# Kernel tuning notes

Hardware: AMD Instinct MI355X
Metric: run time of the kernel (lower is better)

## Reference

```python
import jax, jax.numpy as jnp
import numpy as np

N = 50000


def gcn_conv(x, edge_index, W, b):
    # PyG GCNConv: h = XW; add self-loops; sym-normalized scatter-add; + bias
    n = x.shape[0]
    h = x @ W  # [N, out]
    loop = jnp.arange(n)
    src = jnp.concatenate([edge_index[0], loop])
    dst = jnp.concatenate([edge_index[1], loop])
    deg = jax.ops.segment_sum(jnp.ones_like(dst, dtype=h.dtype), dst, num_segments=n)
    dinv = jax.lax.rsqrt(jnp.maximum(deg, 1.0))  # deg >= 1 after self-loops
    norm = dinv[src] * dinv[dst]  # [E+N]
    msg = h[src] * norm[:, None]  # [E+N, out]
    return jax.ops.segment_sum(msg, dst, num_segments=n) + b


def setup_inputs() -> dict:
    key = jax.random.key(0)
    ks = jax.random.split(key, 20)
    E = 1600000
    inp = {
        "metadata_a": jax.random.normal(ks[0], (N, 512), jnp.float32),
        "metadata_b": jax.random.normal(ks[1], (N, 512), jnp.float32),
        "x_a": jax.random.normal(ks[2], (N, 256), jnp.float32),
        "x_b": jax.random.normal(ks[3], (N, 256), jnp.float32),
        "edge_index_a": jax.random.randint(ks[4], (2, E), 0, N, dtype=jnp.int64),
        "edge_index_b": jax.random.randint(ks[5], (2, E), 0, N, dtype=jnp.int64),
        # parameters (fan-in scaled)
        "fc1_W": jax.random.normal(ks[6], (512, 128), jnp.float32) / np.sqrt(512),
        "fc1_b": jnp.zeros((128,), jnp.float32),
        "fc2_W": jax.random.normal(ks[7], (128, 128), jnp.float32) / np.sqrt(128),
        "fc2_b": jnp.zeros((128,), jnp.float32),
        "gcn1_W": jax.random.normal(ks[8], (256, 128), jnp.float32) / np.sqrt(256),
        "gcn1_b": jnp.zeros((128,), jnp.float32),
        "gcn2_W": jax.random.normal(ks[9], (128, 128), jnp.float32) / np.sqrt(128),
        "gcn2_b": jnp.zeros((128,), jnp.float32),
        "fcc_W": jax.random.normal(ks[10], (512, 128), jnp.float32) / np.sqrt(512),
        "fcc_b": jnp.zeros((128,), jnp.float32),
        "out_W": jax.random.normal(ks[11], (128, 1), jnp.float32) / np.sqrt(128),
        "out_b": jnp.zeros((1,), jnp.float32),
    }
    return inp


def reference(metadata_a, metadata_b, x_a, x_b, edge_index_a, edge_index_b,
              fc1_W, fc1_b, fc2_W, fc2_b, gcn1_W, gcn1_b, gcn2_W, gcn2_b,
              fcc_W, fcc_b, out_W, out_b):
    def mlp(m):
        m = jax.nn.relu(m @ fc1_W + fc1_b)
        return jax.nn.relu(m @ fc2_W + fc2_b)

    def gcn_branch(x, ei):
        x = jax.nn.relu(gcn_conv(x, ei, gcn1_W, gcn1_b))
        return jax.nn.relu(gcn_conv(x, ei, gcn2_W, gcn2_b))

    ma = mlp(metadata_a)
    mb = mlp(metadata_b)
    ga = gcn_branch(x_a, edge_index_a)
    gb = gcn_branch(x_b, edge_index_b)
    combined = jnp.concatenate([ma, mb, ga, gb], axis=1)  # [N, 512]
    combined = jax.nn.relu(combined @ fcc_W + fcc_b)
    return jax.nn.sigmoid(combined @ out_W + out_b)  # [N, 1]
```

## Files before the change

kernel.cpp:

```cpp
#include <hip/hip_runtime.h>
#include <math.h>


typedef __attribute__((ext_vector_type(8))) short bf16x8;
typedef __attribute__((ext_vector_type(4))) float f32x4;

static __device__ __forceinline__ unsigned short f2bf(float f) {
  unsigned u = __float_as_uint(f);
  unsigned r = u + 0x7fffu + ((u >> 16) & 1u);
  return (unsigned short)(r >> 16);
}
static __device__ __forceinline__ float bflo(unsigned m) { return __uint_as_float(m << 16); }
static __device__ __forceinline__ float bfhi(unsigned m) { return __uint_as_float(m & 0xffff0000u); }

static __device__ __forceinline__ bf16x8 cvt8(const float4& l, const float4& h) {
  bf16x8 a;
  a[0] = (short)f2bf(l.x); a[1] = (short)f2bf(l.y);
  a[2] = (short)f2bf(l.z); a[3] = (short)f2bf(l.w);
  a[4] = (short)f2bf(h.x); a[5] = (short)f2bf(h.y);
  a[6] = (short)f2bf(h.z); a[7] = (short)f2bf(h.w);
  return a;
}

template <int AFP32>
__launch_bounds__(256)
__global__ void gemm_mfma(const void* __restrict__ Av, const void* __restrict__ Av2,
                          int lda, const unsigned short* __restrict__ Wt,
                          const float* __restrict__ bias, const float* __restrict__ rowscale,
                          unsigned short* __restrict__ Cb, unsigned short* __restrict__ Cb2,
                          int ldc, int co, int co2, int Mh, int M, int K, int do_relu) {
  const int tid = threadIdx.x;
  const int wave = tid >> 6, lane = tid & 63, quad = lane >> 4, lr = lane & 15;
  const int m0 = blockIdx.x * 64 + wave * 16;

  f32x4 acc[8];
#pragma unroll
  for (int c = 0; c < 8; c++) acc[c] = (f32x4){0.f, 0.f, 0.f, 0.f};

  int rg = m0 + lr; if (rg > M - 1) rg = M - 1;
  const int h = rg >= Mh;
  const size_t rl = (size_t)(rg - (h ? Mh : 0));
  const int KT = K >> 5;

  const bf16x8* Bf = (const bf16x8*)Wt + lane;
  const float* apf = (const float*)(h ? Av2 : Av) + rl * lda + quad * 8;
  const unsigned short* aph = (const unsigned short*)(h ? Av2 : Av) + rl * lda + quad * 8;

  float4 pl[2], ph[2];
  bf16x8 pa[2];
  if (AFP32) {
    pl[0] = *(const float4*)apf; ph[0] = *(const float4*)(apf + 4);
    if (KT > 1) { pl[1] = *(const float4*)(apf + 32); ph[1] = *(const float4*)(apf + 36); }
  } else {
    pa[0] = *(const bf16x8*)aph;
    if (KT > 1) pa[1] = *(const bf16x8*)(aph + 32);
  }
  bf16x8 bc[8], bn[8];
#pragma unroll
  for (int c = 0; c < 8; c++) bc[c] = Bf[c * 64];

  for (int kt = 0; kt < KT; kt++) {
    bf16x8 a;
    if (AFP32) a = cvt8(pl[kt & 1], ph[kt & 1]);
    else       a = pa[kt & 1];
    if (kt + 2 < KT) {
      if (AFP32) {
        const float* pp = apf + (size_t)(kt + 2) * 32;
        pl[kt & 1] = *(const float4*)pp; ph[kt & 1] = *(const float4*)(pp + 4);
      } else {
        pa[kt & 1] = *(const bf16x8*)(aph + (size_t)(kt + 2) * 32);
      }
    }
    if (kt + 1 < KT) {
      const bf16x8* Bk = Bf + (size_t)(kt + 1) * 512;
#pragma unroll
      for (int c = 0; c < 8; c++) bn[c] = Bk[c * 64];
    }
#pragma unroll
    for (int c = 0; c < 8; c++)
      acc[c] = __builtin_amdgcn_mfma_f32_16x16x32_bf16(a, bc[c], acc[c], 0, 0, 0);
    if (kt + 1 < KT) {
#pragma unroll
      for (int c = 0; c < 8; c++) bc[c] = bn[c];
    }
  }

  const int rbase = m0 + quad * 4;
  float rs[4];
#pragma unroll
  for (int i = 0; i < 4; i++) {
    int row = rbase + i;
    rs[i] = (rowscale && row < M) ? rowscale[row] : 1.0f;
  }
#pragma unroll
  for (int c = 0; c < 8; c++) {
    const int nc = c * 16 + lr;
    const float bi = bias ? bias[nc] : 0.f;
#pragma unroll
    for (int i = 0; i < 4; i++) {
      int row = rbase + i;
      if (row < M) {
        int hh = row >= Mh;
        int rr = row - (hh ? Mh : 0);
        float v = acc[c][i] * rs[i] + bi;
        if (do_relu) v = fmaxf(v, 0.f);
        unsigned short* C = hh ? Cb2 : Cb;
        C[(size_t)rr * ldc + (hh ? co2 : co) + nc] = f2bf(v);
      }
    }
  }
}

__launch_bounds__(256)
__global__ void gemm_head(const unsigned short* __restrict__ A,
                          const unsigned short* __restrict__ Wt,
                          const float* __restrict__ bias,
                          const float* __restrict__ outW, const float* __restrict__ outb,
                          float* __restrict__ y, int M) {
  const int tid = threadIdx.x;
  const int wave = tid >> 6, lane = tid & 63, quad = lane >> 4, lr = lane & 15;
  const int m0 = blockIdx.x * 64 + wave * 16;

  f32x4 acc[8];
#pragma unroll
  for (int c = 0; c < 8; c++) acc[c] = (f32x4){0.f, 0.f, 0.f, 0.f};

  int rg = m0 + lr; if (rg > M - 1) rg = M - 1;
  const unsigned short* aph = A + (size_t)rg * 512 + quad * 8;
  const int KT = 16;
  const bf16x8* Bf = (const bf16x8*)Wt + lane;

  bf16x8 pa[2];
  pa[0] = *(const bf16x8*)aph;
  pa[1] = *(const bf16x8*)(aph + 32);
  bf16x8 bc[8], bn[8];
#pragma unroll
  for (int c = 0; c < 8; c++) bc[c] = Bf[c * 64];

  for (int kt = 0; kt < KT; kt++) {
    bf16x8 a = pa[kt & 1];
    if (kt + 2 < KT) pa[kt & 1] = *(const bf16x8*)(aph + (size_t)(kt + 2) * 32);
    if (kt + 1 < KT) {
      const bf16x8* Bk = Bf + (size_t)(kt + 1) * 512;
#pragma unroll
      for (int c = 0; c < 8; c++) bn[c] = Bk[c * 64];
    }
#pragma unroll
    for (int c = 0; c < 8; c++)
      acc[c] = __builtin_amdgcn_mfma_f32_16x16x32_bf16(a, bc[c], acc[c], 0, 0, 0);
    if (kt + 1 < KT) {
#pragma unroll
      for (int c = 0; c < 8; c++) bc[c] = bn[c];
    }
  }

  float part[4] = {0.f, 0.f, 0.f, 0.f};
#pragma unroll
  for (int c = 0; c < 8; c++) {
    const int nc = c * 16 + lr;
    float w = outW[nc];
    float bi = bias[nc];
#pragma unroll
    for (int i = 0; i < 4; i++) part[i] += fmaxf(acc[c][i] + bi, 0.f) * w;
  }
#pragma unroll
  for (int i = 0; i < 4; i++) {
    part[i] += __shfl_xor(part[i], 1, 64);
    part[i] += __shfl_xor(part[i], 2, 64);
    part[i] += __shfl_xor(part[i], 4, 64);
    part[i] += __shfl_xor(part[i], 8, 64);
  }
  if (lr == 0) {
    const float ob = outb[0];
#pragma unroll
    for (int i = 0; i < 4; i++) {
      int row = m0 + quad * 4 + i;
      if (row < M) y[row] = 1.f / (1.f + expf(-(part[i] + ob)));
    }
  }
}

__global__ void prep_w(const float* __restrict__ fc1, const float* __restrict__ fc2,
                       const float* __restrict__ g1, const float* __restrict__ g2,
                       const float* __restrict__ fcc, unsigned short* __restrict__ wt) {
  int t = blockIdx.x * 256 + threadIdx.x;
  const float* src[5] = {fc1, fc2, g1, g2, fcc};
  const int Ks[5] = {512, 128, 256, 128, 512};
  int off = 0;
#pragma unroll
  for (int w = 0; w < 5; w++) {
    int K = Ks[w];
    int ngroups = K * 16;
    if (t < ngroups) {
      int lane = t & 63;
      int c = (t >> 6) & 7;
      int kt = t >> 9;
      int quad = lane >> 4, lr = lane & 15;
      int n = c * 16 + lr;
      unsigned short* dst = wt + off + (size_t)t * 8;
      const float* s = src[w];
#pragma unroll
      for (int j = 0; j < 8; j++) {
        int k = kt * 32 + quad * 8 + j;
        dst[j] = f2bf(s[k * 128 + n]);
      }
    }
    off += K * 128;
  }
}

__global__ void init_csr(int* __restrict__ gcur, int NB, int BCAP) {
  int i = blockIdx.x * 256 + threadIdx.x;
  if (i < 2 * NB) gcur[i] = i * BCAP;
}

__launch_bounds__(256)
__global__ void bucket_scatter(const int* __restrict__ eiA, const int* __restrict__ eiB,
                               int E, int T, int NB, int* __restrict__ gcur,
                               unsigned* __restrict__ records) {
  __shared__ unsigned staging[4096];
  __shared__ int hist[129];
  __shared__ int offs[129];
  __shared__ int gbase[128];
  __shared__ int sm[128];
  const int g = blockIdx.x >= T;
  const int tile = blockIdx.x - g * T;
  const int* ei = g ? eiB : eiA;
  const int tid = threadIdx.x;
  for (int i = tid; i <= NB; i += 256) hist[i] = 0;
  __syncthreads();
  const int base = tile * 4096;
  int myb[16], myp[16];
  unsigned myrec[16];
#pragma unroll
  for (int j = 0; j < 16; j++) {
    int li = base + j * 256 + tid;
    int b = NB;
    unsigned rec = 0;
    if (li < E) {
      int s = ei[li], d = ei[E + li];
      b = d >> 9;
      rec = (unsigned)s | ((unsigned)d << 16);
    }
    myb[j] = b; myrec[j] = rec;
    myp[j] = atomicAdd(&hist[b], 1);
  }
  __syncthreads();
  if (tid < 128) sm[tid] = (tid <= NB) ? hist[tid] : 0;
  __syncthreads();
  for (int d = 1; d < 128; d <<= 1) {
    int v = 0;
    if (tid < 128) { v = sm[tid]; if (tid >= d) v += sm[tid - d]; }
    __syncthreads();
    if (tid < 128) sm[tid] = v;
    __syncthreads();
  }
  if (tid < 128) offs[tid] = sm[tid] - ((tid <= NB) ? hist[tid] : 0);
  __syncthreads();
#pragma unroll
  for (int j = 0; j < 16; j++)
    if (myb[j] < NB) staging[offs[myb[j]] + myp[j]] = myrec[j];
  if (tid < NB && hist[tid] > 0) gbase[tid] = atomicAdd(&gcur[g * NB + tid], hist[tid]);
  __syncthreads();
  const int total = offs[NB];
  for (int i = tid; i < total; i += 256) {
    unsigned rec = staging[i];
    int b = (int)(rec >> 16) >> 9;
    records[gbase[b] + (i - offs[b])] = rec;
  }
}

__launch_bounds__(256)
__global__ void csr_build(const unsigned* __restrict__ records, const int* __restrict__ gcur,
                          int N, int NB, int BCAP,
                          int2* __restrict__ rpA, int2* __restrict__ rpB,
                          float* __restrict__ dinv, unsigned short* __restrict__ csrAll) {
  __shared__ int ncnt[512];
  __shared__ int excl[512];
  __shared__ int sm[256];
  const int g = blockIdx.x >= NB;
  const int b = blockIdx.x - g * NB;
  const int tid = threadIdx.x;
  const int R = (g * NB + b) * BCAP;
  const int cnt = gcur[g * NB + b] - R;
  const int node0 = b << 9;
  const int nb = min(512, N - node0);
  const unsigned* rec = records + R;
  int2* rp = g ? rpB : rpA;
  unsigned short* csr = csrAll + (size_t)g * NB * BCAP;

  for (int i = tid; i < 512; i += 256) ncnt[i] = 0;
  __syncthreads();
  for (int i = tid; i < cnt; i += 256)
    atomicAdd(&ncnt[(rec[i] >> 16) & 511], 1);
  __syncthreads();
  int a0 = ncnt[2 * tid], a1 = ncnt[2 * tid + 1];
  int ps = a0 + a1;
  sm[tid] = ps;
  __syncthreads();
  for (int d = 1; d < 256; d <<= 1) {
    int v = sm[tid];
    if (tid >= d) v += sm[tid - d];
    __syncthreads();
    sm[tid] = v;
    __syncthreads();
  }
  int e0 = sm[tid] - ps;
  excl[2 * tid] = e0;
  excl[2 * tid + 1] = e0 + a0;
  __syncthreads();
  for (int i = tid; i < nb; i += 256) {
    int s = b * BCAP + excl[i];
    rp[node0 + i] = make_int2(s, s + ncnt[i]);
    dinv[g * N + node0 + i] = rsqrtf((float)(ncnt[i] + 1));
  }
  __syncthreads();
  for (int i = tid; i < 512; i += 256) ncnt[i] = excl[i];
  __syncthreads();
  for (int i = tid; i < cnt; i += 256) {
    unsigned r = rec[i];
    int p = atomicAdd(&ncnt[(r >> 16) & 511], 1);
    csr[b * BCAP + p] = (unsigned short)(r & 0xffffu);
  }
}

struct f2x4 { float2 a, b, c, d; };
static __device__ __forceinline__ void acc2(f2x4& A, const uint4& m) {
  A.a.x += bflo(m.x); A.a.y += bfhi(m.x);
  A.b.x += bflo(m.y); A.b.y += bfhi(m.y);
  A.c.x += bflo(m.z); A.c.y += bfhi(m.z);
  A.d.x += bflo(m.w); A.d.y += bfhi(m.w);
}

__launch_bounds__(256)
__global__ void gather16(const unsigned short* __restrict__ hsA,
                         const unsigned short* __restrict__ hsB,
                         const unsigned short* __restrict__ csrA,
                         const unsigned short* __restrict__ csrB,
                         const int2* __restrict__ rpA, const int2* __restrict__ rpB,
                         const float* __restrict__ dinv,
                         const float* __restrict__ bias,
                         unsigned short* __restrict__ outA, unsigned short* __restrict__ outB,
                         int ldA, int coA, int ldB, int coB, int N) {
  int widx = (blockIdx.x * 256 + threadIdx.x) >> 6;
  if (widx >= 2 * N) return;
  int g = widx >= N;
  int v = g ? widx - N : widx;
  const unsigned short* hs = g ? hsB : hsA;
  const unsigned short* csr = g ? csrB : csrA;
  int2 se = (g ? rpB : rpA)[v];
  unsigned short* out = g ? outB : outA;
  const int ldc = g ? ldB : ldA;
  const int co = g ? coB : coA;
  const int lane = threadIdx.x & 63;
  const int grp = lane >> 4;
  const int u = lane & 15;
  const unsigned short* rowb = hs + u * 8;

  f2x4 A0 = {{0,0},{0,0},{0,0},{0,0}};
  f2x4 A1 = {{0,0},{0,0},{0,0},{0,0}};

  int e = se.x;
  const int end = se.y;
  for (; e + 16 <= end; e += 16) {
    int s0 = csr[e + grp];
    int s1 = csr[e + 4 + grp];
    int s2 = csr[e + 8 + grp];
    int s3 = csr[e + 12 + grp];
    uint4 m0 = *(const uint4*)(rowb + (size_t)s0 * 128);
    uint4 m1 = *(const uint4*)(rowb + (size_t)s1 * 128);
    uint4 m2 = *(const uint4*)(rowb + (size_t)s2 * 128);
    uint4 m3 = *(const uint4*)(rowb + (size_t)s3 * 128);
    acc2(A0, m0); acc2(A1, m1); acc2(A0, m2); acc2(A1, m3);
  }
  for (; e + 4 <= end; e += 4) {
    int s0 = csr[e + grp];
    uint4 m0 = *(const uint4*)(rowb + (size_t)s0 * 128);
    acc2(A0, m0);
  }
  int r = end - e;
  if (r > 0) {
    int s0 = csr[e + (grp < r ? grp : r - 1)];
    uint4 m = *(const uint4*)(rowb + (size_t)s0 * 128);
    float msk = (grp < r) ? 1.f : 0.f;
    A1.a.x = fmaf(msk, bflo(m.x), A1.a.x); A1.a.y = fmaf(msk, bfhi(m.x), A1.a.y);
    A1.b.x = fmaf(msk, bflo(m.y), A1.b.x); A1.b.y = fmaf(msk, bfhi(m.y), A1.b.y);
    A1.c.x = fmaf(msk, bflo(m.z), A1.c.x); A1.c.y = fmaf(msk, bfhi(m.z), A1.c.y);
    A1.d.x = fmaf(msk, bflo(m.w), A1.d.x); A1.d.y = fmaf(msk, bfhi(m.w), A1.d.y);
  }

  float acc[8] = {A0.a.x + A1.a.x, A0.a.y + A1.a.y, A0.b.x + A1.b.x, A0.b.y + A1.b.y,
                  A0.c.x + A1.c.x, A0.c.y + A1.c.y, A0.d.x + A1.d.x, A0.d.y + A1.d.y};
#pragma unroll
  for (int j = 0; j < 8; j++) {
    acc[j] += __shfl_down(acc[j], 32, 64);
    acc[j] += __shfl_down(acc[j], 16, 64);
  }
  if (grp == 0) {
    uint4 smv = *(const uint4*)(rowb + (size_t)v * 128);
    acc[0] += bflo(smv.x); acc[1] += bfhi(smv.x);
    acc[2] += bflo(smv.y); acc[3] += bfhi(smv.y);
    acc[4] += bflo(smv.z); acc[5] += bfhi(smv.z);
    acc[6] += bflo(smv.w); acc[7] += bfhi(smv.w);
    float dv = dinv[g * N + v];
    float4 b0 = *(const float4*)(bias + u * 8);
    float4 b1 = *(const float4*)(bias + u * 8 + 4);
    float o0 = fmaxf(acc[0] * dv + b0.x, 0.f), o1 = fmaxf(acc[1] * dv + b0.y, 0.f);
    float o2 = fmaxf(acc[2] * dv + b0.z, 0.f), o3 = fmaxf(acc[3] * dv + b0.w, 0.f);
    float o4 = fmaxf(acc[4] * dv + b1.x, 0.f), o5 = fmaxf(acc[5] * dv + b1.y, 0.f);
    float o6 = fmaxf(acc[6] * dv + b1.z, 0.f), o7 = fmaxf(acc[7] * dv + b1.w, 0.f);
    uint4 P;
    P.x = (unsigned)f2bf(o0) | ((unsigned)f2bf(o1) << 16);
    P.y = (unsigned)f2bf(o2) | ((unsigned)f2bf(o3) << 16);
    P.z = (unsigned)f2bf(o4) | ((unsigned)f2bf(o5) << 16);
    P.w = (unsigned)f2bf(o6) | ((unsigned)f2bf(o7) << 16);
    *(uint4*)(out + (size_t)v * ldc + co + u * 8) = P;
  }
}

extern "C" void kernel_launch(void* const* d_in, const int* in_sizes, int n_in,
                              void* d_out, int out_size, void* d_ws, size_t ws_size,
                              hipStream_t stream) {
  const float* meta_a = (const float*)d_in[0];
  const float* meta_b = (const float*)d_in[1];
  const float* x_a    = (const float*)d_in[2];
  const float* x_b    = (const float*)d_in[3];
  const int*   ei_a   = (const int*)d_in[4];
  const int*   ei_b   = (const int*)d_in[5];
  const float* fc1_W = (const float*)d_in[6];
  const float* fc1_b = (const float*)d_in[7];
  const float* fc2_W = (const float*)d_in[8];
  const float* fc2_b = (const float*)d_in[9];
  const float* gcn1_W = (const float*)d_in[10];
  const float* gcn1_b = (const float*)d_in[11];
  const float* gcn2_W = (const float*)d_in[12];
  const float* gcn2_b = (const float*)d_in[13];
  const float* fcc_W = (const float*)d_in[14];
  const float* fcc_b = (const float*)d_in[15];
  const float* out_W = (const float*)d_in[16];
  const float* out_b = (const float*)d_in[17];
  float* y = (float*)d_out;

  const int N = in_sizes[0] / 512;
  const int E = in_sizes[4] / 2;
  const int NB = (N + 511) >> 9;
  const int T = (E + 4095) / 4096;
  const int BCAP = 17408;

  char* p = (char*)d_ws;
  auto alloc = [&](size_t bytes) { char* r = p; p += (bytes + 255) & ~255ull; return r; };
  unsigned short* combined = (unsigned short*)alloc((size_t)N * 512 * 2);
  unsigned short* t0 = (unsigned short*)alloc((size_t)N * 128 * 2);
  unsigned short* t1 = (unsigned short*)alloc((size_t)N * 128 * 2);
  unsigned short* t2 = (unsigned short*)alloc((size_t)N * 128 * 2);
  unsigned short* t3 = (unsigned short*)alloc((size_t)N * 128 * 2);
  unsigned short* wt = (unsigned short*)alloc(196608 * 2);
  float* dinv = (float*)alloc((size_t)2 * N * 4);
  int2* rpA = (int2*)alloc((size_t)N * 8);
  int2* rpB = (int2*)alloc((size_t)N * 8);
  int* gcur = (int*)alloc((size_t)2 * NB * 4);
  unsigned* records = (unsigned*)alloc((size_t)2 * NB * BCAP * 4 + 4096);
  unsigned short* csrAll = (unsigned short*)alloc((size_t)2 * NB * BCAP * 2 + 4096);
  unsigned short* csrA = csrAll;
  unsigned short* csrB = csrAll + (size_t)NB * BCAP;

  unsigned short* wt_fc1 = wt;
  unsigned short* wt_fc2 = wt + 65536;
  unsigned short* wt_g1  = wt + 81920;
  unsigned short* wt_g2  = wt + 114688;
  unsigned short* wt_fcc = wt + 131072;

  const int grid1 = (N + 63) / 64;
  const int grid2 = (2 * N + 63) / 64;

  prep_w<<<32, 256, 0, stream>>>(fc1_W, fc2_W, gcn1_W, gcn2_W, fcc_W, wt);
  init_csr<<<1, 256, 0, stream>>>(gcur, NB, BCAP);
  bucket_scatter<<<2 * T, 256, 0, stream>>>(ei_a, ei_b, E, T, NB, gcur, records);
  csr_build<<<2 * NB, 256, 0, stream>>>(records, gcur, N, NB, BCAP, rpA, rpB, dinv, csrAll);

  gemm_mfma<1><<<grid2, 256, 0, stream>>>(meta_a, meta_b, 512, wt_fc1, fc1_b, nullptr,
                                          t0, t1, 128, 0, 0, N, 2 * N, 512, 1);
  gemm_mfma<0><<<grid2, 256, 0, stream>>>(t0, t1, 128, wt_fc2, fc2_b, nullptr,
                                          combined, combined, 512, 0, 128, N, 2 * N, 128, 1);

  gemm_mfma<1><<<grid2, 256, 0, stream>>>(x_a, x_b, 256, wt_g1, nullptr, dinv,
                                          t0, t1, 128, 0, 0, N, 2 * N, 256, 0);
  gather16<<<(2 * N + 3) / 4, 256, 0, stream>>>(t0, t1, csrA, csrB, rpA, rpB, dinv, gcn1_b,
                                                t2, t3, 128, 0, 128, 0, N);
  gemm_mfma<0><<<grid2, 256, 0, stream>>>(t2, t3, 128, wt_g2, nullptr, dinv,
                                          t0, t1, 128, 0, 0, N, 2 * N, 128, 0);
  gather16<<<(2 * N + 3) / 4, 256, 0, stream>>>(t0, t1, csrA, csrB, rpA, rpB, dinv, gcn2_b,
                                                combined, combined, 512, 256, 512, 384, N);

  gemm_head<<<grid1, 256, 0, stream>>>(combined, wt_fcc, fcc_b, out_W, out_b, y, N);
}
```

Measured before the change: 808.2 us.

## Stage GEMM weights in LDS via async loads and double the rows per wave

Both GEMM kernels now copy each 32-wide K slice of the weight matrix into a double-buffered shared-memory tile using global_load_lds, instead of having every wave load it from global memory into registers. Each wave now computes two 16-row tiles against the same weight fragment, so a block covers 128 rows and the grids are halved. The aim is to cut redundant weight traffic and increase MFMA work per weight load. In exchange it adds a block-wide barrier every K step and roughly doubles accumulator register use, which may lower occupancy.

```diff
diff --git a/kernel.cpp b/kernel.cpp
--- a/kernel.cpp
+++ b/kernel.cpp
@@ -22,6 +22,12 @@
   return a;
 }
 
+static __device__ __forceinline__ void gl_lds16(const unsigned short* g, unsigned short* l) {
+  __builtin_amdgcn_global_load_lds(
+      (const __attribute__((address_space(1))) void*)g,
+      (__attribute__((address_space(3))) void*)l, 16, 0, 0);
+}
+
 template <int AFP32>
 __launch_bounds__(256)
 __global__ void gemm_mfma(const void* __restrict__ Av, const void* __restrict__ Av2,
@@ -29,83 +35,106 @@
                           const float* __restrict__ bias, const float* __restrict__ rowscale,
                           unsigned short* __restrict__ Cb, unsigned short* __restrict__ Cb2,
                           int ldc, int co, int co2, int Mh, int M, int K, int do_relu) {
+  __shared__ unsigned short Bs[2][4096];
   const int tid = threadIdx.x;
   const int wave = tid >> 6, lane = tid & 63, quad = lane >> 4, lr = lane & 15;
-  const int m0 = blockIdx.x * 64 + wave * 16;
-
-  f32x4 acc[8];
-#pragma unroll
-  for (int c = 0; c < 8; c++) acc[c] = (f32x4){0.f, 0.f, 0.f, 0.f};
-
-  int rg = m0 + lr; if (rg > M - 1) rg = M - 1;
-  const int h = rg >= Mh;
-  const size_t rl = (size_t)(rg - (h ? Mh : 0));
+  const int m0 = blockIdx.x * 128 + wave * 32;
   const int KT = K >> 5;
 
-  const bf16x8* Bf = (const bf16x8*)Wt + lane;
-  const float* apf = (const float*)(h ? Av2 : Av) + rl * lda + quad * 8;
-  const unsigned short* aph = (const unsigned short*)(h ? Av2 : Av) + rl * lda + quad * 8;
-
-  float4 pl[2], ph[2];
-  bf16x8 pa[2];
-  if (AFP32) {
-    pl[0] = *(const float4*)apf; ph[0] = *(const float4*)(apf + 4);
-    if (KT > 1) { pl[1] = *(const float4*)(apf + 32); ph[1] = *(const float4*)(apf + 36); }
-  } else {
-    pa[0] = *(const bf16x8*)aph;
-    if (KT > 1) pa[1] = *(const bf16x8*)(aph + 32);
-  }
-  bf16x8 bc[8], bn[8];
-#pragma unroll
-  for (int c = 0; c < 8; c++) bc[c] = Bf[c * 64];
-
+  f32x4 acc[2][8];
+#pragma unroll
+  for (int t = 0; t < 2; t++)
+#pragma unroll
+    for (int c = 0; c < 8; c++) acc[t][c] = (f32x4){0.f, 0.f, 0.f, 0.f};
+
+  const float* apf[2];
+  const unsigned short* aph[2];
+#pragma unroll
+  for (int t = 0; t < 2; t++) {
+    int rg = m0 + t * 16 + lr; if (rg > M - 1) rg = M - 1;
+    const int h = rg >= Mh;
+    const size_t rl = (size_t)(rg - (h ? Mh : 0));
+    if (AFP32) apf[t] = (const float*)(h ? Av2 : Av) + rl * lda + quad * 8;
+    else       aph[t] = (const unsigned short*)(h ? Av2 : Av) + rl * lda + quad * 8;
+  }
+
+  {
+    const unsigned short* g = Wt + wave * 1024 + lane * 8;
+    gl_lds16(g,       &Bs[0][wave * 1024]);
+    gl_lds16(g + 512, &Bs[0][wave * 1024 + 512]);
+  }
+  float4 pl[2][2], ph[2][2];
+  bf16x8 pa[2][2];
+#pragma unroll
+  for (int t = 0; t < 2; t++) {
+    if (AFP32) {
+      pl[t][0] = *(const float4*)apf[t]; ph[t][0] = *(const float4*)(apf[t] + 4);
+      if (KT > 1) { pl[t][1] = *(const float4*)(apf[t] + 32); ph[t][1] = *(const float4*)(apf[t] + 36); }
+    } else {
+      pa[t][0] = *(const bf16x8*)aph[t];
+      if (KT > 1) pa[t][1] = *(const bf16x8*)(aph[t] + 32);
+    }
+  }
+  __syncthreads();
+
+  int buf = 0;
   for (int kt = 0; kt < KT; kt++) {
-    bf16x8 a;
-    if (AFP32) a = cvt8(pl[kt & 1], ph[kt & 1]);
-    else       a = pa[kt & 1];
+    if (kt + 1 < KT) {
+      const unsigned short* g = Wt + (size_t)(kt + 1) * 4096 + wave * 1024 + lane * 8;
+      gl_lds16(g,       &Bs[buf ^ 1][wave * 1024]);
+      gl_lds16(g + 512, &Bs[buf ^ 1][wave * 1024 + 512]);
+    }
+    bf16x8 a[2];
+#pragma unroll
+    for (int t = 0; t < 2; t++) {
+      if (AFP32) a[t] = cvt8(pl[t][kt & 1], ph[t][kt & 1]);
+      else       a[t] = pa[t][kt & 1];
+    }
     if (kt + 2 < KT) {
-      if (AFP32) {
-        const float* pp = apf + (size_t)(kt + 2) * 32;
-        pl[kt & 1] = *(const float4*)pp; ph[kt & 1] = *(const float4*)(pp + 4);
-      } else {
-        pa[kt & 1] = *(const bf16x8*)(aph + (size_t)(kt + 2) * 32);
+#pragma unroll
+      for (int t = 0; t < 2; t++) {
+        if (AFP32) {
+          const float* pp = apf[t] + (size_t)(kt + 2) * 32;
+          pl[t][kt & 1] = *(const float4*)pp; ph[t][kt & 1] = *(const float4*)(pp + 4);
+        } else {
+          pa[t][kt & 1] = *(const bf16x8*)(aph[t] + (size_t)(kt + 2) * 32);
+        }
       }
     }
-    if (kt + 1 < KT) {
-      const bf16x8* Bk = Bf + (size_t)(kt + 1) * 512;
-#pragma unroll
-      for (int c = 0; c < 8; c++) bn[c] = Bk[c * 64];
-    }
-#pragma unroll
-    for (int c = 0; c < 8; c++)
-      acc[c] = __builtin_amdgcn_mfma_f32_16x16x32_bf16(a, bc[c], acc[c], 0, 0, 0);
-    if (kt + 1 < KT) {
-#pragma unroll
-      for (int c = 0; c < 8; c++) bc[c] = bn[c];
-    }
-  }
-
-  const int rbase = m0 + quad * 4;
-  float rs[4];
-#pragma unroll
-  for (int i = 0; i < 4; i++) {
-    int row = rbase + i;
-    rs[i] = (rowscale && row < M) ? rowscale[row] : 1.0f;
-  }
-#pragma unroll
-  for (int c = 0; c < 8; c++) {
-    const int nc = c * 16 + lr;
-    const float bi = bias ? bias[nc] : 0.f;
+#pragma unroll
+    for (int c = 0; c < 8; c++) {
+      bf16x8 b = *(const bf16x8*)&Bs[buf][(c * 64 + lane) * 8];
+      acc[0][c] = __builtin_amdgcn_mfma_f32_16x16x32_bf16(a[0], b, acc[0][c], 0, 0, 0);
+      acc[1][c] = __builtin_amdgcn_mfma_f32_16x16x32_bf16(a[1], b, acc[1][c], 0, 0, 0);
+    }
+    if (kt + 1 < KT) __syncthreads();
+    buf ^= 1;
+  }
+
+#pragma unroll
+  for (int t = 0; t < 2; t++) {
+    const int rbase = m0 + t * 16 + quad * 4;
+    float rs[4];
 #pragma unroll
     for (int i = 0; i < 4; i++) {
       int row = rbase + i;
-      if (row < M) {
-        int hh = row >= Mh;
-        int rr = row - (hh ? Mh : 0);
-        float v = acc[c][i] * rs[i] + bi;
-        if (do_relu) v = fmaxf(v, 0.f);
-        unsigned short* C = hh ? Cb2 : Cb;
-        C[(size_t)rr * ldc + (hh ? co2 : co) + nc] = f2bf(v);
+      rs[i] = (rowscale && row < M) ? rowscale[row] : 1.0f;
+    }
+#pragma unroll
+    for (int c = 0; c < 8; c++) {
+      const int nc = c * 16 + lr;
+      const float bi = bias ? bias[nc] : 0.f;
+#pragma unroll
+      for (int i = 0; i < 4; i++) {
+        int row = rbase + i;
+        if (row < M) {
+          int hh = row >= Mh;
+          int rr = row - (hh ? Mh : 0);
+          float v = acc[t][c][i] * rs[i] + bi;
+          if (do_relu) v = fmaxf(v, 0.f);
+          unsigned short* C = hh ? Cb2 : Cb;
+          C[(size_t)rr * ldc + (hh ? co2 : co) + nc] = f2bf(v);
+        }
       }
     }
   }
@@ -117,66 +146,92 @@
                           const float* __restrict__ bias,
                           const float* __restrict__ outW, const float* __restrict__ outb,
                           float* __restrict__ y, int M) {
+  __shared__ unsigned short Bs[2][4096];
   const int tid = threadIdx.x;
   const int wave = tid >> 6, lane = tid & 63, quad = lane >> 4, lr = lane & 15;
-  const int m0 = blockIdx.x * 64 + wave * 16;
-
-  f32x4 acc[8];
-#pragma unroll
-  for (int c = 0; c < 8; c++) acc[c] = (f32x4){0.f, 0.f, 0.f, 0.f};
-
-  int rg = m0 + lr; if (rg > M - 1) rg = M - 1;
-  const unsigned short* aph = A + (size_t)rg * 512 + quad * 8;
+  const int m0 = blockIdx.x * 128 + wave * 32;
   const int KT = 16;
-  const bf16x8* Bf = (const bf16x8*)Wt + lane;
-
-  bf16x8 pa[2];
-  pa[0] = *(const bf16x8*)aph;
-  pa[1] = *(const bf16x8*)(aph + 32);
-  bf16x8 bc[8], bn[8];
-#pragma unroll
-  for (int c = 0; c < 8; c++) bc[c] = Bf[c * 64];
-
+
+  f32x4 acc[2][8];
+#pragma unroll
+  for (int t = 0; t < 2; t++)
+#pragma unroll
+    for (int c = 0; c < 8; c++) acc[t][c] = (f32x4){0.f, 0.f, 0.f, 0.f};
+
+  const unsigned short* aph[2];
+#pragma unroll
+  for (int t = 0; t < 2; t++) {
+    int rg = m0 + t * 16 + lr; if (rg > M - 1) rg = M - 1;
+    aph[t] = A + (size_t)rg * 512 + quad * 8;
+  }
+
+  {
+    const unsigned short* g = Wt + wave * 1024 + lane * 8;
+    gl_lds16(g,       &Bs[0][wave * 1024]);
+    gl_lds16(g + 512, &Bs[0][wave * 1024 + 512]);
+  }
+  bf16x8 pa[2][2];
+#pragma unroll
+  for (int t = 0; t < 2; t++) {
+    pa[t][0] = *(const bf16x8*)aph[t];
+    pa[t][1] = *(const bf16x8*)(aph[t] + 32);
+  }
+  __syncthreads();
+
+  int buf = 0;
   for (int kt = 0; kt < KT; kt++) {
-    bf16x8 a = pa[kt & 1];
-    if (kt + 2 < KT) pa[kt & 1] = *(const bf16x8*)(aph + (size_t)(kt + 2) * 32);
     if (kt + 1 < KT) {
-      const bf16x8* Bk = Bf + (size_t)(kt + 1) * 512;
-#pragma unroll
-      for (int c = 0; c < 8; c++) bn[c] = Bk[c * 64];
-    }
-#pragma unroll
-    for (int c = 0; c < 8; c++)
-      acc[c] = __builtin_amdgcn_mfma_f32_16x16x32_bf16(a, bc[c], acc[c], 0, 0, 0);
-    if (kt + 1 < KT) {
-#pragma unroll
-      for (int c = 0; c < 8; c++) bc[c] = bn[c];
-    }
-  }
-
-  float part[4] = {0.f, 0.f, 0.f, 0.f};
-#pragma unroll
-  for (int c = 0; c < 8; c++) {
-    const int nc = c * 16 + lr;
-    float w = outW[nc];
-    float bi = bias[nc];
-#pragma unroll
-    for (int i = 0; i < 4; i++) part[i] += fmaxf(acc[c][i] + bi, 0.f) * w;
-  }
-#pragma unroll
-  for (int i = 0; i < 4; i++) {
-    part[i] += __shfl_xor(part[i], 1, 64);
-    part[i] += __shfl_xor(part[i], 2, 64);
-    part[i] += __shfl_xor(part[i], 4, 64);
-    part[i] += __shfl_xor(part[i], 8, 64);
-  }
+      const unsigned short* g = Wt + (size_t)(kt + 1) * 4096 + wave * 1024 + lane * 8;
+      gl_lds16(g,       &Bs[buf ^ 1][wave * 1024]);
+      gl_lds16(g + 512, &Bs[buf ^ 1][wave * 1024 + 512]);
+    }
+    bf16x8 a[2];
+#pragma unroll
+    for (int t = 0; t < 2; t++) a[t] = pa[t][kt & 1];
+    if (kt + 2 < KT) {
+#pragma unroll
+      for (int t = 0; t < 2; t++)
+        pa[t][kt & 1] = *(const bf16x8*)(aph[t] + (size_t)(kt + 2) * 32);
+    }
+#pragma unroll
+    for (int c = 0; c < 8; c++) {
+      bf16x8 b = *(const bf16x8*)&Bs[buf][(c * 64 + lane) * 8];
+      acc[0][c] = __builtin_amdgcn_mfma_f32_16x16x32_bf16(a[0], b, acc[0][c], 0, 0, 0);
+      acc[1][c] = __builtin_amdgcn_mfma_f32_16x16x32_bf16(a[1], b, acc[1][c], 0, 0, 0);
+    }
+    if (kt + 1 < KT) __syncthreads();
+    buf ^= 1;
+  }
+
+  float part[2][4] = {{0.f, 0.f, 0.f, 0.f}, {0.f, 0.f, 0.f, 0.f}};
+#pragma unroll
+  for (int t = 0; t < 2; t++)
+#pragma unroll
+    for (int c = 0; c < 8; c++) {
+      const int nc = c * 16 + lr;
+      float w = outW[nc];
+      float bi = bias[nc];
+#pragma unroll
+      for (int i = 0; i < 4; i++) part[t][i] += fmaxf(acc[t][c][i] + bi, 0.f) * w;
+    }
+#pragma unroll
+  for (int t = 0; t < 2; t++)
+#pragma unroll
+    for (int i = 0; i < 4; i++) {
+      part[t][i] += __shfl_xor(part[t][i], 1, 64);
+      part[t][i] += __shfl_xor(part[t][i], 2, 64);
+      part[t][i] += __shfl_xor(part[t][i], 4, 64);
+      part[t][i] += __shfl_xor(part[t][i], 8, 64);
+    }
   if (lr == 0) {
     const float ob = outb[0];
 #pragma unroll
-    for (int i = 0; i < 4; i++) {
-      int row = m0 + quad * 4 + i;
-      if (row < M) y[row] = 1.f / (1.f + expf(-(part[i] + ob)));
-    }
+    for (int t = 0; t < 2; t++)
+#pragma unroll
+      for (int i = 0; i < 4; i++) {
+        int row = m0 + t * 16 + quad * 4 + i;
+        if (row < M) y[row] = 1.f / (1.f + expf(-(part[t][i] + ob)));
+      }
   }
 }
 
@@ -470,8 +525,8 @@
   unsigned short* wt_g2  = wt + 114688;
   unsigned short* wt_fcc = wt + 131072;
 
-  const int grid1 = (N + 63) / 64;
-  const int grid2 = (2 * N + 63) / 64;
+  const int grid1 = (N + 127) / 128;
+  const int grid2 = (2 * N + 127) / 128;
 
   prep_w<<<32, 256, 0, stream>>>(fc1_W, fc2_W, gcn1_W, gcn2_W, fcc_W, wt);
   init_csr<<<1, 256, 0, stream>>>(gcur, NB, BCAP);
```

After: 965.5 us. 1.19x slower.

## Stage fp32 GEMM inputs through LDS with direct global-to-LDS loads

Applied to the files above, without the earlier changes.

The fp32-input GEMMs (fc1 and gcn1) now stage the A tile into double-buffered shared memory with global_load_lds, using an XOR swizzle, and read it back for bf16 conversion, instead of each lane issuing strided per-row register loads. The K=128 bf16 GEMMs get a specialised kernel that preloads all four A fragments up front. The head GEMM now prefetches A in groups of four k-steps. The aim is better-coalesced, deeper-pipelined reads of the large fp32 activation matrices, at the cost of 64KB of shared memory per block (lower occupancy) and a block barrier per chunk.

```diff
diff --git a/kernel.cpp b/kernel.cpp
--- a/kernel.cpp
+++ b/kernel.cpp
@@ -22,66 +22,86 @@
   return a;
 }
 
-template <int AFP32>
+static __device__ __forceinline__ void gl_lds16(const unsigned short* g, unsigned short* l) {
+  __builtin_amdgcn_global_load_lds(
+      (const __attribute__((address_space(1))) void*)g,
+      (__attribute__((address_space(3))) void*)l, 16, 0, 0);
+}
+
+template <int KT>
 __launch_bounds__(256)
-__global__ void gemm_mfma(const void* __restrict__ Av, const void* __restrict__ Av2,
-                          int lda, const unsigned short* __restrict__ Wt,
-                          const float* __restrict__ bias, const float* __restrict__ rowscale,
-                          unsigned short* __restrict__ Cb, unsigned short* __restrict__ Cb2,
-                          int ldc, int co, int co2, int Mh, int M, int K, int do_relu) {
+__global__ void gemm_staged(const float* __restrict__ Av, const float* __restrict__ Av2,
+                            int lda, const unsigned short* __restrict__ Wt,
+                            const float* __restrict__ bias, const float* __restrict__ rowscale,
+                            unsigned short* __restrict__ Cb, unsigned short* __restrict__ Cb2,
+                            int ldc, int co, int co2, int Mh, int M, int do_relu) {
+  static_assert(KT % 4 == 0, "KT multiple of 4");
+  constexpr int NCH = KT / 4;
+  __shared__ float4 As[2][2048];
   const int tid = threadIdx.x;
   const int wave = tid >> 6, lane = tid & 63, quad = lane >> 4, lr = lane & 15;
   const int m0 = blockIdx.x * 64 + wave * 16;
+  const int mb = blockIdx.x * 64;
 
   f32x4 acc[8];
 #pragma unroll
   for (int c = 0; c < 8; c++) acc[c] = (f32x4){0.f, 0.f, 0.f, 0.f};
 
-  int rg = m0 + lr; if (rg > M - 1) rg = M - 1;
-  const int h = rg >= Mh;
-  const size_t rl = (size_t)(rg - (h ? Mh : 0));
-  const int KT = K >> 5;
+  const int colq_src = (tid & 7) ^ ((tid >> 3) & 7);
+  int r0g = mb + (tid >> 3);      if (r0g > M - 1) r0g = M - 1;
+  int r1g = mb + 32 + (tid >> 3); if (r1g > M - 1) r1g = M - 1;
+  const int h0 = r0g >= Mh, h1 = r1g >= Mh;
+  const float* srcb0 = (h0 ? Av2 : Av) + (size_t)(r0g - (h0 ? Mh : 0)) * lda + colq_src * 4;
+  const float* srcb1 = (h1 ? Av2 : Av) + (size_t)(r1g - (h1 ? Mh : 0)) * lda + colq_src * 4;
+
+  auto stage = [&](int buf, int c0) {
+#pragma unroll
+    for (int s = 0; s < 8; s++) {
+      const float* g = ((s & 1) ? srcb1 : srcb0) + (size_t)(c0 * 4 + (s >> 1)) * 32;
+      gl_lds16((const unsigned short*)g,
+               (unsigned short*)&As[buf][s * 256 + wave * 64]);
+    }
+  };
+
+  const int h32 = wave >> 1;
+  const int r5 = (wave & 1) * 16 + lr;
+  const int swz = r5 & 7;
+  const int fb_ = h32 * 256 + r5 * 8;
 
   const bf16x8* Bf = (const bf16x8*)Wt + lane;
-  const float* apf = (const float*)(h ? Av2 : Av) + rl * lda + quad * 8;
-  const unsigned short* aph = (const unsigned short*)(h ? Av2 : Av) + rl * lda + quad * 8;
-
-  float4 pl[2], ph[2];
-  bf16x8 pa[2];
-  if (AFP32) {
-    pl[0] = *(const float4*)apf; ph[0] = *(const float4*)(apf + 4);
-    if (KT > 1) { pl[1] = *(const float4*)(apf + 32); ph[1] = *(const float4*)(apf + 36); }
-  } else {
-    pa[0] = *(const bf16x8*)aph;
-    if (KT > 1) pa[1] = *(const bf16x8*)(aph + 32);
-  }
-  bf16x8 bc[8], bn[8];
-#pragma unroll
-  for (int c = 0; c < 8; c++) bc[c] = Bf[c * 64];
-
-  for (int kt = 0; kt < KT; kt++) {
-    bf16x8 a;
-    if (AFP32) a = cvt8(pl[kt & 1], ph[kt & 1]);
-    else       a = pa[kt & 1];
-    if (kt + 2 < KT) {
-      if (AFP32) {
-        const float* pp = apf + (size_t)(kt + 2) * 32;
-        pl[kt & 1] = *(const float4*)pp; ph[kt & 1] = *(const float4*)(pp + 4);
-      } else {
-        pa[kt & 1] = *(const bf16x8*)(aph + (size_t)(kt + 2) * 32);
+
+  stage(0, 0);
+  bf16x8 bb[2][8];
+#pragma unroll
+  for (int c = 0; c < 8; c++) bb[0][c] = Bf[c * 64];
+  __builtin_amdgcn_sched_barrier(0);
+  asm volatile("s_waitcnt vmcnt(0)" ::: "memory");
+  __builtin_amdgcn_s_barrier();
+  __builtin_amdgcn_sched_barrier(0);
+
+  for (int ch = 0; ch < NCH; ch++) {
+    if (ch + 1 < NCH) stage((ch + 1) & 1, ch + 1);
+    const float4* cur = As[ch & 1];
+#pragma unroll
+    for (int kk = 0; kk < 4; kk++) {
+      const int kt = ch * 4 + kk;
+      float4 f0 = cur[kk * 512 + fb_ + ((2 * quad) ^ swz)];
+      float4 f1 = cur[kk * 512 + fb_ + ((2 * quad + 1) ^ swz)];
+      bf16x8 a = cvt8(f0, f1);
+      if (kt + 1 < KT) {
+        const bf16x8* Bk = Bf + (size_t)(kt + 1) * 512;
+#pragma unroll
+        for (int c = 0; c < 8; c++) bb[(kk + 1) & 1][c] = Bk[c * 64];
       }
-    }
-    if (kt + 1 < KT) {
-      const bf16x8* Bk = Bf + (size_t)(kt + 1) * 512;
-#pragma unroll
-      for (int c = 0; c < 8; c++) bn[c] = Bk[c * 64];
-    }
-#pragma unroll
-    for (int c = 0; c < 8; c++)
-      acc[c] = __builtin_amdgcn_mfma_f32_16x16x32_bf16(a, bc[c], acc[c], 0, 0, 0);
-    if (kt + 1 < KT) {
-#pragma unroll
-      for (int c = 0; c < 8; c++) bc[c] = bn[c];
+#pragma unroll
+      for (int c = 0; c < 8; c++)
+        acc[c] = __builtin_amdgcn_mfma_f32_16x16x32_bf16(a, bb[kk & 1][c], acc[c], 0, 0, 0);
+    }
+    if (ch + 1 < NCH) {
+      __builtin_amdgcn_sched_barrier(0);
+      asm volatile("s_waitcnt vmcnt(0)" ::: "memory");
+      __builtin_amdgcn_s_barrier();
+      __builtin_amdgcn_sched_barrier(0);
     }
   }
 
@@ -112,11 +132,77 @@
 }
 
 __launch_bounds__(256)
+__global__ void gemm_reg4(const unsigned short* __restrict__ Av, const unsigned short* __restrict__ Av2,
+                          int lda, const unsigned short* __restrict__ Wt,
+                          const float* __restrict__ bias, const float* __restrict__ rowscale,
+                          unsigned short* __restrict__ Cb, unsigned short* __restrict__ Cb2,
+                          int ldc, int co, int co2, int Mh, int M, int do_relu) {
+  const int tid = threadIdx.x;
+  const int wave = tid >> 6, lane = tid & 63, quad = lane >> 4, lr = lane & 15;
+  const int m0 = blockIdx.x * 64 + wave * 16;
+
+  f32x4 acc[8];
+#pragma unroll
+  for (int c = 0; c < 8; c++) acc[c] = (f32x4){0.f, 0.f, 0.f, 0.f};
+
+  int rg = m0 + lr; if (rg > M - 1) rg = M - 1;
+  const int h = rg >= Mh;
+  const unsigned short* aph = (h ? Av2 : Av) + (size_t)(rg - (h ? Mh : 0)) * lda + quad * 8;
+  const bf16x8* Bf = (const bf16x8*)Wt + lane;
+
+  bf16x8 hb[4];
+#pragma unroll
+  for (int k = 0; k < 4; k++) hb[k] = *(const bf16x8*)(aph + (size_t)k * 32);
+
+  bf16x8 bb[2][8];
+#pragma unroll
+  for (int c = 0; c < 8; c++) bb[0][c] = Bf[c * 64];
+
+#pragma unroll
+  for (int kt = 0; kt < 4; kt++) {
+    if (kt + 1 < 4) {
+      const bf16x8* Bk = Bf + (size_t)(kt + 1) * 512;
+#pragma unroll
+      for (int c = 0; c < 8; c++) bb[(kt + 1) & 1][c] = Bk[c * 64];
+    }
+#pragma unroll
+    for (int c = 0; c < 8; c++)
+      acc[c] = __builtin_amdgcn_mfma_f32_16x16x32_bf16(hb[kt], bb[kt & 1][c], acc[c], 0, 0, 0);
+  }
+
+  const int rbase = m0 + quad * 4;
+  float rs[4];
+#pragma unroll
+  for (int i = 0; i < 4; i++) {
+    int row = rbase + i;
+    rs[i] = (rowscale && row < M) ? rowscale[row] : 1.0f;
+  }
+#pragma unroll
+  for (int c = 0; c < 8; c++) {
+    const int nc = c * 16 + lr;
+    const float bi = bias ? bias[nc] : 0.f;
+#pragma unroll
+    for (int i = 0; i < 4; i++) {
+      int row = rbase + i;
+      if (row < M) {
+        int hh = row >= Mh;
+        int rr = row - (hh ? Mh : 0);
+        float v = acc[c][i] * rs[i] + bi;
+        if (do_relu) v = fmaxf(v, 0.f);
+        unsigned short* C = hh ? Cb2 : Cb;
+        C[(size_t)rr * ldc + (hh ? co2 : co) + nc] = f2bf(v);
+      }
+    }
+  }
+}
+
+__launch_bounds__(256)
 __global__ void gemm_head(const unsigned short* __restrict__ A,
                           const unsigned short* __restrict__ Wt,
                           const float* __restrict__ bias,
                           const float* __restrict__ outW, const float* __restrict__ outb,
                           float* __restrict__ y, int M) {
+  constexpr int KT = 16;
   const int tid = threadIdx.x;
   const int wave = tid >> 6, lane = tid & 63, quad = lane >> 4, lr = lane & 15;
   const int m0 = blockIdx.x * 64 + wave * 16;
@@ -127,32 +213,40 @@
 
   int rg = m0 + lr; if (rg > M - 1) rg = M - 1;
   const unsigned short* aph = A + (size_t)rg * 512 + quad * 8;
-  const int KT = 16;
   const bf16x8* Bf = (const bf16x8*)Wt + lane;
 
-  bf16x8 pa[2];
-  pa[0] = *(const bf16x8*)aph;
-  pa[1] = *(const bf16x8*)(aph + 32);
-  bf16x8 bc[8], bn[8];
-#pragma unroll
-  for (int c = 0; c < 8; c++) bc[c] = Bf[c * 64];
-
-  for (int kt = 0; kt < KT; kt++) {
-    bf16x8 a = pa[kt & 1];
-    if (kt + 2 < KT) pa[kt & 1] = *(const bf16x8*)(aph + (size_t)(kt + 2) * 32);
-    if (kt + 1 < KT) {
-      const bf16x8* Bk = Bf + (size_t)(kt + 1) * 512;
-#pragma unroll
-      for (int c = 0; c < 8; c++) bn[c] = Bk[c * 64];
-    }
-#pragma unroll
-    for (int c = 0; c < 8; c++)
-      acc[c] = __builtin_amdgcn_mfma_f32_16x16x32_bf16(a, bc[c], acc[c], 0, 0, 0);
-    if (kt + 1 < KT) {
-#pragma unroll
-      for (int c = 0; c < 8; c++) bc[c] = bn[c];
-    }
-  }
+  bf16x8 hb[2][4];
+#define LOADH(SLOT, BT)                                                     \
+  if ((BT) < 4) {                                                           \
+    _Pragma("unroll")                                                       \
+    for (int kk = 0; kk < 4; kk++)                                          \
+      hb[SLOT][kk] = *(const bf16x8*)(aph + (size_t)((BT) * 4 + kk) * 32);  \
+  }
+  LOADH(0, 0)
+  LOADH(1, 1)
+
+  bf16x8 bb[2][8];
+#pragma unroll
+  for (int c = 0; c < 8; c++) bb[0][c] = Bf[c * 64];
+
+#pragma unroll
+  for (int bt = 0; bt < 4; bt++) {
+#pragma unroll
+    for (int kk = 0; kk < 4; kk++) {
+      const int kt = bt * 4 + kk;
+      bf16x8 a = hb[bt & 1][kk];
+      if (kt + 1 < KT) {
+        const bf16x8* Bk = Bf + (size_t)(kt + 1) * 512;
+#pragma unroll
+        for (int c = 0; c < 8; c++) bb[(kk + 1) & 1][c] = Bk[c * 64];
+      }
+      if (kk == 3) { LOADH(bt & 1, bt + 2) }
+#pragma unroll
+      for (int c = 0; c < 8; c++)
+        acc[c] = __builtin_amdgcn_mfma_f32_16x16x32_bf16(a, bb[kk & 1][c], acc[c], 0, 0, 0);
+    }
+  }
+#undef LOADH
 
   float part[4] = {0.f, 0.f, 0.f, 0.f};
 #pragma unroll
@@ -478,17 +572,17 @@
   bucket_scatter<<<2 * T, 256, 0, stream>>>(ei_a, ei_b, E, T, NB, gcur, records);
   csr_build<<<2 * NB, 256, 0, stream>>>(records, gcur, N, NB, BCAP, rpA, rpB, dinv, csrAll);
 
-  gemm_mfma<1><<<grid2, 256, 0, stream>>>(meta_a, meta_b, 512, wt_fc1, fc1_b, nullptr,
-                                          t0, t1, 128, 0, 0, N, 2 * N, 512, 1);
-  gemm_mfma<0><<<grid2, 256, 0, stream>>>(t0, t1, 128, wt_fc2, fc2_b, nullptr,
-                                          combined, combined, 512, 0, 128, N, 2 * N, 128, 1);
-
-  gemm_mfma<1><<<grid2, 256, 0, stream>>>(x_a, x_b, 256, wt_g1, nullptr, dinv,
-                                          t0, t1, 128, 0, 0, N, 2 * N, 256, 0);
+  gemm_staged<16><<<grid2, 256, 0, stream>>>(meta_a, meta_b, 512, wt_fc1, fc1_b, nullptr,
+                                             t0, t1, 128, 0, 0, N, 2 * N, 1);
+  gemm_reg4<<<grid2, 256, 0, stream>>>(t0, t1, 128, wt_fc2, fc2_b, nullptr,
+                                       combined, combined, 512, 0, 128, N, 2 * N, 1);
+
+  gemm_staged<8><<<grid2, 256, 0, stream>>>(x_a, x_b, 256, wt_g1, nullptr, dinv,
+                                            t0, t1, 128, 0, 0, N, 2 * N, 0);
   gather16<<<(2 * N + 3) / 4, 256, 0, stream>>>(t0, t1, csrA, csrB, rpA, rpB, dinv, gcn1_b,
                                                 t2, t3, 128, 0, 128, 0, N);
-  gemm_mfma<0><<<grid2, 256, 0, stream>>>(t2, t3, 128, wt_g2, nullptr, dinv,
-                                          t0, t1, 128, 0, 0, N, 2 * N, 128, 0);
+  gemm_reg4<<<grid2, 256, 0, stream>>>(t2, t3, 128, wt_g2, nullptr, dinv,
+                                       t0, t1, 128, 0, 0, N, 2 * N, 0);
   gather16<<<(2 * N + 3) / 4, 256, 0, stream>>>(t0, t1, csrA, csrB, rpA, rpB, dinv, gcn2_b,
                                                 combined, combined, 512, 256, 512, 384, N);
 
```

Measured after the change: 745.8 us. 7.7% less time.
